# Kernel optimization log

Hardware: AMD Instinct MI355X
Metric: run time of the kernel (lower is better)

## Reference

```python
import jax, jax.numpy as jnp
import numpy as np

N, T, E = 20000, 4, 320000
IN_F, H_F, OUT_F, HEADS = 32, 16, 16, 8
NEG_SLOPE = 0.2


def gat_layer(x, W, al, ar, b, src, dst, n_nodes, heads, f_out):
    # x: [N, T, Fin], W: [Fin, heads*f_out], al/ar: [heads, f_out], b: [heads*f_out]
    feat = (x @ W).reshape(x.shape[0], x.shape[1], heads, f_out)      # [N,T,H,F]
    el = (feat * al).sum(-1)                                          # [N,T,H]
    er = (feat * ar).sum(-1)                                          # [N,T,H]
    e = jax.nn.leaky_relu(el[src] + er[dst], NEG_SLOPE)               # [E,T,H]
    # segment softmax over incoming edges of each destination node
    m = jax.lax.stop_gradient(jax.ops.segment_max(e, dst, num_segments=n_nodes))
    ex = jnp.exp(e - m[dst])
    s = jax.ops.segment_sum(ex, dst, num_segments=n_nodes)
    alpha = ex / s[dst]                                               # [E,T,H]
    msg = feat[src] * alpha[..., None]                                # [E,T,H,F]
    out = jax.ops.segment_sum(msg, dst, num_segments=n_nodes)
    return out + b.reshape(1, 1, heads, f_out)


def setup_inputs() -> dict:
    key = jax.random.key(0)
    ks = jax.random.split(key, 12)
    x = jax.random.normal(ks[0], (N, T, IN_F), dtype=jnp.float32)
    src = jax.random.randint(ks[1], (E,), 0, N)
    dst = jax.random.randint(ks[2], (E,), 0, N)
    s = 0.1
    W1 = jax.random.normal(ks[3], (IN_F, HEADS * H_F), dtype=jnp.float32) * s
    al1 = jax.random.normal(ks[4], (HEADS, H_F), dtype=jnp.float32) * s
    ar1 = jax.random.normal(ks[5], (HEADS, H_F), dtype=jnp.float32) * s
    b1 = jnp.zeros((HEADS * H_F,), dtype=jnp.float32)
    W2 = jax.random.normal(ks[6], (HEADS * H_F, OUT_F), dtype=jnp.float32) * s
    al2 = jax.random.normal(ks[7], (1, OUT_F), dtype=jnp.float32) * s
    ar2 = jax.random.normal(ks[8], (1, OUT_F), dtype=jnp.float32) * s
    b2 = jnp.zeros((OUT_F,), dtype=jnp.float32)
    return {"x": x, "src": src, "dst": dst, "W1": W1, "al1": al1, "ar1": ar1,
            "b1": b1, "W2": W2, "al2": al2, "ar2": ar2, "b2": b2}


def reference(x, src, dst, W1, al1, ar1, b1, W2, al2, ar2, b2):
    n = x.shape[0]
    h = gat_layer(x, W1, al1, ar1, b1, src, dst, n, HEADS, H_F)   # [N,T,H,F]
    h = h.reshape(n, h.shape[1], -1)                              # [N,T,H*F]
    h = gat_layer(h, W2, al2, ar2, b2, src, dst, n, 1, OUT_F)     # [N,T,1,OUT]
    return h.squeeze(2)                                           # [N,T,OUT]
```

## Files before the change

kernel.cpp:

```cpp
#include <hip/hip_runtime.h>
#include <hip/hip_fp16.h>
#include <math.h>

#define NN 20000
#define TT 4
#define EE 320000
#define NT (NN*TT)
#define H1 8
#define C1 128
#define IN_F 32
#define OUT_F 16
#define CAP 96

typedef _Float16 h8 __attribute__((ext_vector_type(8)));
typedef _Float16 h4v __attribute__((ext_vector_type(4)));
typedef float f32x4 __attribute__((ext_vector_type(4)));

__device__ __forceinline__ float lrelu_exp(float e) {
  e = (e >= 0.f) ? e : 0.2f * e;
  return __expf(e);
}

__global__ __launch_bounds__(256) void k_scatter_prep(
    const int4* __restrict__ src4, const int4* __restrict__ dst4,
    int* __restrict__ cnt, int* __restrict__ csr96,
    const float* __restrict__ W1, const float* __restrict__ al1,
    const float* __restrict__ ar1, const float* __restrict__ W2,
    const float* __restrict__ al2, const float* __restrict__ ar2,
    __half* __restrict__ W1p, __half* __restrict__ W2p) {
  int tid = threadIdx.x;
  int e4 = blockIdx.x * 256 + tid;
  if (e4 < EE / 4) {
    int4 s = src4[e4];
    int4 d = dst4[e4];
    int p0 = atomicAdd(&cnt[d.x], 1); csr96[d.x * CAP + p0] = s.x;
    int p1 = atomicAdd(&cnt[d.y], 1); csr96[d.y * CAP + p1] = s.y;
    int p2 = atomicAdd(&cnt[d.z], 1); csr96[d.z * CAP + p2] = s.z;
    int p3 = atomicAdd(&cnt[d.w], 1); csr96[d.w * CAP + p3] = s.w;
  }
  if (blockIdx.x == 0) {
    for (int idx = tid; idx < 9 * 512; idx += 256) {
      int tile = idx >> 9;
      int rem = idx & 511;
      int lane = rem >> 3, j = rem & 7;
      int k = (lane >> 4) * 8 + j;
      int n = lane & 15;
      float v;
      if (tile < 8) {
        v = W1[k * C1 + tile * 16 + n];
      } else {
        int hh = n & 7;
        const float* a = (n < 8) ? al1 : ar1;
        float s = 0.f;
        for (int f = 0; f < 16; ++f) s += W1[k * C1 + hh * 16 + f] * a[hh * 16 + f];
        v = s;
      }
      W1p[idx] = __float2half(v);
    }
    for (int idx = tid; idx < 8 * 512; idx += 256) {
      int tile = idx >> 9;
      int rem = idx & 511;
      int lane = rem >> 3, j = rem & 7;
      int ks = tile & 3;
      int k = ks * 32 + (lane >> 4) * 8 + j;
      int n = lane & 15;
      float v = 0.f;
      if (tile < 4) {
        v = W2[k * OUT_F + n];
      } else if (n == 0) {
        float s = 0.f;
        for (int f = 0; f < 16; ++f) s += W2[k * OUT_F + f] * al2[f];
        v = s;
      } else if (n == 1) {
        float s = 0.f;
        for (int f = 0; f < 16; ++f) s += W2[k * OUT_F + f] * ar2[f];
        v = s;
      }
      W2p[idx] = __float2half(v);
    }
  }
}

__global__ __launch_bounds__(256) void k_feat1(
    const float* __restrict__ x, const __half* __restrict__ W1p,
    __half* __restrict__ feat1h, float* __restrict__ el1, float* __restrict__ er1) {
  int tid = threadIdx.x;
  int wave = tid >> 6, lane = tid & 63;
  int m = lane & 15, quad = lane >> 4;
  int rowbase = blockIdx.x * 64 + wave * 16;
  int row = rowbase + m;
  const float4* xp = (const float4*)(x + row * IN_F + quad * 8);
  float4 a0 = xp[0], a1 = xp[1];
  h8 af;
  af[0] = (_Float16)a0.x; af[1] = (_Float16)a0.y;
  af[2] = (_Float16)a0.z; af[3] = (_Float16)a0.w;
  af[4] = (_Float16)a1.x; af[5] = (_Float16)a1.y;
  af[6] = (_Float16)a1.z; af[7] = (_Float16)a1.w;
  const h8* bp = (const h8*)W1p;
#pragma unroll
  for (int ht = 0; ht < 8; ++ht) {
    h8 bf = bp[ht * 64 + lane];
    f32x4 c = {0.f, 0.f, 0.f, 0.f};
    c = __builtin_amdgcn_mfma_f32_16x16x32_f16(af, bf, c, 0, 0, 0);
#pragma unroll
    for (int r = 0; r < 4; ++r)
      feat1h[(size_t)(rowbase + quad * 4 + r) * C1 + ht * 16 + m] = __float2half(c[r]);
  }
  {
    h8 bf = bp[8 * 64 + lane];
    f32x4 c = {0.f, 0.f, 0.f, 0.f};
    c = __builtin_amdgcn_mfma_f32_16x16x32_f16(af, bf, c, 0, 0, 0);
#pragma unroll
    for (int r = 0; r < 4; ++r) {
      int orow = rowbase + quad * 4 + r;
      if (m < 8) el1[orow * H1 + m] = c[r];
      else       er1[orow * H1 + (m - 8)] = c[r];
    }
  }
}

__global__ __launch_bounds__(256) void k_agg1(
    const __half* __restrict__ feat1h,
    const float* __restrict__ el1,
    const float* __restrict__ er1,
    const int* __restrict__ cnt, const int* __restrict__ csr96,
    const float* __restrict__ b1, __half* __restrict__ hh) {
  int tid = threadIdx.x;
  int wv = tid >> 6, lane = tid & 63;
  int n = blockIdx.x * 4 + wv;
  int ci = lane & 15;
  int i32 = lane & 31;
  int src_lane = ((lane >> 4) << 3) + (ci >> 1);
  float er_i = er1[(size_t)n * 32 + i32];
  int deg = cnt[n];
  const int* eb = csr96 + (size_t)n * CAP;
  float acc[8];
#pragma unroll
  for (int k = 0; k < 8; ++k) acc[k] = 0.f;
  float l = 0.f;
  for (int chunk = 0; chunk < deg; chunk += 64) {
    int m = min(64, deg - chunk);
    int sv = (lane < m) ? eb[chunk + lane] : 0;
    int iters = (m + 7) >> 3;
    for (int g = 0; g < iters; ++g) {
      int j = g * 8;
      int s0 = __builtin_amdgcn_readlane(sv, j + 0);
      int s1 = __builtin_amdgcn_readlane(sv, j + 1);
      int s2 = __builtin_amdgcn_readlane(sv, j + 2);
      int s3 = __builtin_amdgcn_readlane(sv, j + 3);
      int s4 = __builtin_amdgcn_readlane(sv, j + 4);
      int s5 = __builtin_amdgcn_readlane(sv, j + 5);
      int s6 = __builtin_amdgcn_readlane(sv, j + 6);
      int s7 = __builtin_amdgcn_readlane(sv, j + 7);
      float ew0 = el1[(size_t)s0 * 32 + i32];
      float ew1 = el1[(size_t)s1 * 32 + i32];
      float ew2 = el1[(size_t)s2 * 32 + i32];
      float ew3 = el1[(size_t)s3 * 32 + i32];
      float ew4 = el1[(size_t)s4 * 32 + i32];
      float ew5 = el1[(size_t)s5 * 32 + i32];
      float ew6 = el1[(size_t)s6 * 32 + i32];
      float ew7 = el1[(size_t)s7 * 32 + i32];
      h8 f0 = *(const h8*)(feat1h + (size_t)s0 * 512 + lane * 8);
      h8 f1 = *(const h8*)(feat1h + (size_t)s1 * 512 + lane * 8);
      h8 f2 = *(const h8*)(feat1h + (size_t)s2 * 512 + lane * 8);
      h8 f3 = *(const h8*)(feat1h + (size_t)s3 * 512 + lane * 8);
      h8 f4 = *(const h8*)(feat1h + (size_t)s4 * 512 + lane * 8);
      h8 f5 = *(const h8*)(feat1h + (size_t)s5 * 512 + lane * 8);
      h8 f6 = *(const h8*)(feat1h + (size_t)s6 * 512 + lane * 8);
      h8 f7 = *(const h8*)(feat1h + (size_t)s7 * 512 + lane * 8);
#define CONSUME(K, EW, F)                                         \
      {                                                           \
        float w_ = lrelu_exp(EW + er_i);                          \
        w_ = (j + K < m) ? w_ : 0.f;                              \
        float wb_ = __shfl(w_, src_lane);                         \
        l += wb_;                                                 \
        _Pragma("unroll")                                         \
        for (int q = 0; q < 8; ++q)                               \
          acc[q] = fmaf(wb_, (float)F[q], acc[q]);                \
      }
      CONSUME(0, ew0, f0) CONSUME(1, ew1, f1)
      CONSUME(2, ew2, f2) CONSUME(3, ew3, f3)
      CONSUME(4, ew4, f4) CONSUME(5, ew5, f5)
      CONSUME(6, ew6, f6) CONSUME(7, ew7, f7)
#undef CONSUME
    }
  }
  float inv = (l > 0.f) ? (1.f / l) : 0.f;
  float4 bv0 = *(const float4*)&b1[ci * 8];
  float4 bv1 = *(const float4*)&b1[ci * 8 + 4];
  h8 r;
  r[0] = (_Float16)(acc[0] * inv + bv0.x);
  r[1] = (_Float16)(acc[1] * inv + bv0.y);
  r[2] = (_Float16)(acc[2] * inv + bv0.z);
  r[3] = (_Float16)(acc[3] * inv + bv0.w);
  r[4] = (_Float16)(acc[4] * inv + bv1.x);
  r[5] = (_Float16)(acc[5] * inv + bv1.y);
  r[6] = (_Float16)(acc[6] * inv + bv1.z);
  r[7] = (_Float16)(acc[7] * inv + bv1.w);
  *(h8*)(hh + (size_t)n * 512 + lane * 8) = r;
}

__global__ __launch_bounds__(256) void k_feat2(
    const __half* __restrict__ hh, const __half* __restrict__ W2p,
    __half* __restrict__ feat2h, float* __restrict__ el2, float* __restrict__ er2) {
  int tid = threadIdx.x;
  int wave = tid >> 6, lane = tid & 63;
  int m = lane & 15, quad = lane >> 4;
  int rowbase = blockIdx.x * 64 + wave * 16;
  const h8* hp = (const h8*)hh;
  const h8* bp = (const h8*)W2p;
  f32x4 cF = {0.f, 0.f, 0.f, 0.f};
  f32x4 cE = {0.f, 0.f, 0.f, 0.f};
#pragma unroll
  for (int ks = 0; ks < 4; ++ks) {
    h8 af = hp[(size_t)(rowbase + m) * 16 + ks * 4 + quad];
    cF = __builtin_amdgcn_mfma_f32_16x16x32_f16(af, bp[ks * 64 + lane], cF, 0, 0, 0);
    cE = __builtin_amdgcn_mfma_f32_16x16x32_f16(af, bp[(4 + ks) * 64 + lane], cE, 0, 0, 0);
  }
#pragma unroll
  for (int r = 0; r < 4; ++r) {
    int orow = rowbase + quad * 4 + r;
    feat2h[(size_t)orow * OUT_F + m] = __float2half(cF[r]);
    if (m == 0) el2[orow] = cE[r];
    if (m == 1) er2[orow] = cE[r];
  }
}

__global__ __launch_bounds__(256) void k_agg2(
    const __half* __restrict__ feat2h,
    const float* __restrict__ el2, const float* __restrict__ er2,
    const int* __restrict__ cnt, const int* __restrict__ csr96,
    const float* __restrict__ b2, float* __restrict__ out) {
  __shared__ float myp[4][64][5];
  __shared__ int   svs[4][64];
  int tid = threadIdx.x;
  int wv = tid >> 6, lane = tid & 63;
  int n = blockIdx.x * 4 + wv;
  int e4 = lane >> 4, sub = lane & 15;
  int t = sub >> 2, fq = sub & 3;
  int deg = cnt[n];
  const int* eb = csr96 + (size_t)n * CAP;
  float4 ern = *(const float4*)&er2[n * TT];
  float acc[4] = {0.f, 0.f, 0.f, 0.f};
  float l = 0.f;
  for (int chunk = 0; chunk < deg; chunk += 64) {
    int m = min(64, deg - chunk);
    float4 w = {0.f, 0.f, 0.f, 0.f};
    int s = 0;
    if (lane < m) {
      s = eb[chunk + lane];
      float4 e = *(const float4*)&el2[s * TT];
      w.x = lrelu_exp(e.x + ern.x);
      w.y = lrelu_exp(e.y + ern.y);
      w.z = lrelu_exp(e.z + ern.z);
      w.w = lrelu_exp(e.w + ern.w);
    }
    svs[wv][lane] = s;
    myp[wv][lane][0] = w.x;
    myp[wv][lane][1] = w.y;
    myp[wv][lane][2] = w.z;
    myp[wv][lane][3] = w.w;
    int iters = (m + 3) >> 2;
    for (int g = 0; g < iters; ++g) {
      int jb = g * 4;
      int se = svs[wv][jb + e4];
      float we = myp[wv][jb + e4][t];
      h4v fv = *(const h4v*)(feat2h + (size_t)se * 64 + t * 16 + fq * 4);
      l += we;
      acc[0] = fmaf(we, (float)fv[0], acc[0]);
      acc[1] = fmaf(we, (float)fv[1], acc[1]);
      acc[2] = fmaf(we, (float)fv[2], acc[2]);
      acc[3] = fmaf(we, (float)fv[3], acc[3]);
    }
  }
#pragma unroll
  for (int mask = 16; mask <= 32; mask <<= 1) {
#pragma unroll
    for (int k = 0; k < 4; ++k) acc[k] += __shfl_xor(acc[k], mask);
    l += __shfl_xor(l, mask);
  }
  if (e4 == 0) {
    float inv = (l > 0.f) ? (1.f / l) : 0.f;
    float4 r;
    r.x = acc[0] * inv + b2[fq * 4 + 0];
    r.y = acc[1] * inv + b2[fq * 4 + 1];
    r.z = acc[2] * inv + b2[fq * 4 + 2];
    r.w = acc[3] * inv + b2[fq * 4 + 3];
    *(float4*)&out[(size_t)(n * TT + t) * OUT_F + fq * 4] = r;
  }
}

extern "C" void kernel_launch(void* const* d_in, const int* in_sizes, int n_in,
                              void* d_out, int out_size, void* d_ws, size_t ws_size,
                              hipStream_t stream) {
  const float* x   = (const float*)d_in[0];
  const int*   src = (const int*)d_in[1];
  const int*   dst = (const int*)d_in[2];
  const float* W1  = (const float*)d_in[3];
  const float* al1 = (const float*)d_in[4];
  const float* ar1 = (const float*)d_in[5];
  const float* b1  = (const float*)d_in[6];
  const float* W2  = (const float*)d_in[7];
  const float* al2 = (const float*)d_in[8];
  const float* ar2 = (const float*)d_in[9];
  const float* b2  = (const float*)d_in[10];
  float* out = (float*)d_out;

  char* w = (char*)d_ws;
  __half* feat1h = (__half*)w; w += (size_t)NT * C1 * 2;
  __half* hh     = (__half*)w; w += (size_t)NT * C1 * 2;
  __half* feat2h = (__half*)w; w += (size_t)NT * OUT_F * 2;
  float*  el1    = (float*)w;  w += (size_t)NT * H1 * 4;
  float*  er1    = (float*)w;  w += (size_t)NT * H1 * 4;
  float*  el2    = (float*)w;  w += (size_t)NT * 4;
  float*  er2    = (float*)w;  w += (size_t)NT * 4;
  __half* W1p    = (__half*)w; w += (size_t)9 * 512 * 2;
  __half* W2p    = (__half*)w; w += (size_t)8 * 512 * 2;
  int* cnt     = (int*)w;      w += (size_t)NN * 4;
  int* csr96   = (int*)w;      w += (size_t)NN * CAP * 4;

  hipMemsetAsync(cnt, 0, NN * sizeof(int), stream);

  k_scatter_prep<<<(EE / 4 + 255) / 256, 256, 0, stream>>>(
      (const int4*)src, (const int4*)dst, cnt, csr96,
      W1, al1, ar1, W2, al2, ar2, W1p, W2p);
  k_feat1<<<NT / 64, 256, 0, stream>>>(x, W1p, feat1h, el1, er1);
  k_agg1<<<NN / 4, 256, 0, stream>>>(feat1h, el1, er1, cnt, csr96, b1, hh);
  k_feat2<<<NT / 64, 256, 0, stream>>>(hh, W2p, feat2h, el2, er2);
  k_agg2<<<NN / 4, 256, 0, stream>>>(feat2h, el2, er2, cnt, csr96, b2, out);
}
```

Baseline: 181.0 us.

## Fuse edge scatter with layer-1 projection and fold layer-2 projection into aggregation

Merges the CSR scatter and the layer-1 feature projection into one launch, with blocks split by index, and has each block build packed W1 in shared memory. Folds the layer-2 projection into the layer-1 aggregation kernel: each wave keeps its node's hidden row in registers, shuffles it into MFMA operand layout and writes feat2/el2/er2 directly. This removes two kernel launches and the full 128-channel fp16 hidden-state round trip through global memory. In exchange every block recomputes the packed weight matrices, which adds redundant work and shared-memory use per block.

```diff
diff --git a/kernel.cpp b/kernel.cpp
--- a/kernel.cpp
+++ b/kernel.cpp
@@ -11,52 +11,108 @@
 #define IN_F 32
 #define OUT_F 16
 #define CAP 96
+#define SCAT_BLOCKS 313
+#define FEAT1_BLOCKS 1250
 
 typedef _Float16 h8 __attribute__((ext_vector_type(8)));
 typedef _Float16 h4v __attribute__((ext_vector_type(4)));
 typedef float f32x4 __attribute__((ext_vector_type(4)));
+typedef int i4v __attribute__((ext_vector_type(4)));
 
 __device__ __forceinline__ float lrelu_exp(float e) {
   e = (e >= 0.f) ? e : 0.2f * e;
   return __expf(e);
 }
 
-__global__ __launch_bounds__(256) void k_scatter_prep(
+__global__ __launch_bounds__(256) void k_front(
+    const float* __restrict__ x, const float* __restrict__ W1,
+    const float* __restrict__ al1, const float* __restrict__ ar1,
     const int4* __restrict__ src4, const int4* __restrict__ dst4,
     int* __restrict__ cnt, int* __restrict__ csr96,
-    const float* __restrict__ W1, const float* __restrict__ al1,
-    const float* __restrict__ ar1, const float* __restrict__ W2,
-    const float* __restrict__ al2, const float* __restrict__ ar2,
-    __half* __restrict__ W1p, __half* __restrict__ W2p) {
+    __half* __restrict__ feat1h, float* __restrict__ el1,
+    float* __restrict__ er1) {
+  __shared__ h8 W1ps[9 * 64];
+  int b = blockIdx.x;
   int tid = threadIdx.x;
-  int e4 = blockIdx.x * 256 + tid;
-  if (e4 < EE / 4) {
-    int4 s = src4[e4];
-    int4 d = dst4[e4];
-    int p0 = atomicAdd(&cnt[d.x], 1); csr96[d.x * CAP + p0] = s.x;
-    int p1 = atomicAdd(&cnt[d.y], 1); csr96[d.y * CAP + p1] = s.y;
-    int p2 = atomicAdd(&cnt[d.z], 1); csr96[d.z * CAP + p2] = s.z;
-    int p3 = atomicAdd(&cnt[d.w], 1); csr96[d.w * CAP + p3] = s.w;
-  }
-  if (blockIdx.x == 0) {
-    for (int idx = tid; idx < 9 * 512; idx += 256) {
-      int tile = idx >> 9;
-      int rem = idx & 511;
-      int lane = rem >> 3, j = rem & 7;
-      int k = (lane >> 4) * 8 + j;
-      int n = lane & 15;
-      float v;
-      if (tile < 8) {
-        v = W1[k * C1 + tile * 16 + n];
-      } else {
-        int hh = n & 7;
-        const float* a = (n < 8) ? al1 : ar1;
-        float s = 0.f;
-        for (int f = 0; f < 16; ++f) s += W1[k * C1 + hh * 16 + f] * a[hh * 16 + f];
-        v = s;
-      }
-      W1p[idx] = __float2half(v);
-    }
+  if (b < SCAT_BLOCKS) {
+    int e4 = b * 256 + tid;
+    if (e4 < EE / 4) {
+      int4 s = src4[e4];
+      int4 d = dst4[e4];
+      int p0 = atomicAdd(&cnt[d.x], 1); csr96[d.x * CAP + p0] = s.x;
+      int p1 = atomicAdd(&cnt[d.y], 1); csr96[d.y * CAP + p1] = s.y;
+      int p2 = atomicAdd(&cnt[d.z], 1); csr96[d.z * CAP + p2] = s.z;
+      int p3 = atomicAdd(&cnt[d.w], 1); csr96[d.w * CAP + p3] = s.w;
+    }
+    return;
+  }
+  __half* W1p = (__half*)W1ps;
+  for (int idx = tid; idx < 9 * 512; idx += 256) {
+    int tile = idx >> 9;
+    int rem = idx & 511;
+    int lane = rem >> 3, j = rem & 7;
+    int k = (lane >> 4) * 8 + j;
+    int n = lane & 15;
+    float v;
+    if (tile < 8) {
+      v = W1[k * C1 + tile * 16 + n];
+    } else {
+      int hh_ = n & 7;
+      const float* a = (n < 8) ? al1 : ar1;
+      float s = 0.f;
+      for (int f = 0; f < 16; ++f) s += W1[k * C1 + hh_ * 16 + f] * a[hh_ * 16 + f];
+      v = s;
+    }
+    W1p[idx] = __float2half(v);
+  }
+  __syncthreads();
+  int wave = tid >> 6, lane = tid & 63;
+  int m = lane & 15, quad = lane >> 4;
+  int rowbase = (b - SCAT_BLOCKS) * 64 + wave * 16;
+  int row = rowbase + m;
+  const float4* xp = (const float4*)(x + row * IN_F + quad * 8);
+  float4 a0 = xp[0], a1 = xp[1];
+  h8 af;
+  af[0] = (_Float16)a0.x; af[1] = (_Float16)a0.y;
+  af[2] = (_Float16)a0.z; af[3] = (_Float16)a0.w;
+  af[4] = (_Float16)a1.x; af[5] = (_Float16)a1.y;
+  af[6] = (_Float16)a1.z; af[7] = (_Float16)a1.w;
+#pragma unroll
+  for (int ht = 0; ht < 8; ++ht) {
+    h8 bf = W1ps[ht * 64 + lane];
+    f32x4 c = {0.f, 0.f, 0.f, 0.f};
+    c = __builtin_amdgcn_mfma_f32_16x16x32_f16(af, bf, c, 0, 0, 0);
+#pragma unroll
+    for (int r = 0; r < 4; ++r)
+      feat1h[(size_t)(rowbase + quad * 4 + r) * C1 + ht * 16 + m] = __float2half(c[r]);
+  }
+  {
+    h8 bf = W1ps[8 * 64 + lane];
+    f32x4 c = {0.f, 0.f, 0.f, 0.f};
+    c = __builtin_amdgcn_mfma_f32_16x16x32_f16(af, bf, c, 0, 0, 0);
+#pragma unroll
+    for (int r = 0; r < 4; ++r) {
+      int orow = rowbase + quad * 4 + r;
+      if (m < 8) el1[orow * H1 + m] = c[r];
+      else       er1[orow * H1 + (m - 8)] = c[r];
+    }
+  }
+}
+
+__global__ __launch_bounds__(256) void k_agg1f(
+    const __half* __restrict__ feat1h,
+    const float* __restrict__ el1,
+    const float* __restrict__ er1,
+    const int* __restrict__ cnt, const int* __restrict__ csr96,
+    const float* __restrict__ b1,
+    const float* __restrict__ W2, const float* __restrict__ al2,
+    const float* __restrict__ ar2,
+    __half* __restrict__ feat2h, float* __restrict__ el2,
+    float* __restrict__ er2) {
+  __shared__ h8 W2ps[8 * 64];
+  int tid = threadIdx.x;
+  {
+    __half* W2p = (__half*)W2ps;
     for (int idx = tid; idx < 8 * 512; idx += 256) {
       int tile = idx >> 9;
       int rem = idx & 511;
@@ -79,53 +135,8 @@
       W2p[idx] = __float2half(v);
     }
   }
-}
-
-__global__ __launch_bounds__(256) void k_feat1(
-    const float* __restrict__ x, const __half* __restrict__ W1p,
-    __half* __restrict__ feat1h, float* __restrict__ el1, float* __restrict__ er1) {
-  int tid = threadIdx.x;
-  int wave = tid >> 6, lane = tid & 63;
-  int m = lane & 15, quad = lane >> 4;
-  int rowbase = blockIdx.x * 64 + wave * 16;
-  int row = rowbase + m;
-  const float4* xp = (const float4*)(x + row * IN_F + quad * 8);
-  float4 a0 = xp[0], a1 = xp[1];
-  h8 af;
-  af[0] = (_Float16)a0.x; af[1] = (_Float16)a0.y;
-  af[2] = (_Float16)a0.z; af[3] = (_Float16)a0.w;
-  af[4] = (_Float16)a1.x; af[5] = (_Float16)a1.y;
-  af[6] = (_Float16)a1.z; af[7] = (_Float16)a1.w;
-  const h8* bp = (const h8*)W1p;
-#pragma unroll
-  for (int ht = 0; ht < 8; ++ht) {
-    h8 bf = bp[ht * 64 + lane];
-    f32x4 c = {0.f, 0.f, 0.f, 0.f};
-    c = __builtin_amdgcn_mfma_f32_16x16x32_f16(af, bf, c, 0, 0, 0);
-#pragma unroll
-    for (int r = 0; r < 4; ++r)
-      feat1h[(size_t)(rowbase + quad * 4 + r) * C1 + ht * 16 + m] = __float2half(c[r]);
-  }
-  {
-    h8 bf = bp[8 * 64 + lane];
-    f32x4 c = {0.f, 0.f, 0.f, 0.f};
-    c = __builtin_amdgcn_mfma_f32_16x16x32_f16(af, bf, c, 0, 0, 0);
-#pragma unroll
-    for (int r = 0; r < 4; ++r) {
-      int orow = rowbase + quad * 4 + r;
-      if (m < 8) el1[orow * H1 + m] = c[r];
-      else       er1[orow * H1 + (m - 8)] = c[r];
-    }
-  }
-}
-
-__global__ __launch_bounds__(256) void k_agg1(
-    const __half* __restrict__ feat1h,
-    const float* __restrict__ el1,
-    const float* __restrict__ er1,
-    const int* __restrict__ cnt, const int* __restrict__ csr96,
-    const float* __restrict__ b1, __half* __restrict__ hh) {
-  int tid = threadIdx.x;
+  __syncthreads();
+
   int wv = tid >> 6, lane = tid & 63;
   int n = blockIdx.x * 4 + wv;
   int ci = lane & 15;
@@ -197,32 +208,33 @@
   r[5] = (_Float16)(acc[5] * inv + bv1.y);
   r[6] = (_Float16)(acc[6] * inv + bv1.z);
   r[7] = (_Float16)(acc[7] * inv + bv1.w);
-  *(h8*)(hh + (size_t)n * 512 + lane * 8) = r;
-}
-
-__global__ __launch_bounds__(256) void k_feat2(
-    const __half* __restrict__ hh, const __half* __restrict__ W2p,
-    __half* __restrict__ feat2h, float* __restrict__ el2, float* __restrict__ er2) {
-  int tid = threadIdx.x;
-  int wave = tid >> 6, lane = tid & 63;
+
+  union U { h8 v; i4v d; };
+  U u; u.v = r;
   int m = lane & 15, quad = lane >> 4;
-  int rowbase = blockIdx.x * 64 + wave * 16;
-  const h8* hp = (const h8*)hh;
-  const h8* bp = (const h8*)W2p;
   f32x4 cF = {0.f, 0.f, 0.f, 0.f};
   f32x4 cE = {0.f, 0.f, 0.f, 0.f};
 #pragma unroll
   for (int ks = 0; ks < 4; ++ks) {
-    h8 af = hp[(size_t)(rowbase + m) * 16 + ks * 4 + quad];
-    cF = __builtin_amdgcn_mfma_f32_16x16x32_f16(af, bp[ks * 64 + lane], cF, 0, 0, 0);
-    cE = __builtin_amdgcn_mfma_f32_16x16x32_f16(af, bp[(4 + ks) * 64 + lane], cE, 0, 0, 0);
-  }
-#pragma unroll
-  for (int r = 0; r < 4; ++r) {
-    int orow = rowbase + quad * 4 + r;
-    feat2h[(size_t)orow * OUT_F + m] = __float2half(cF[r]);
-    if (m == 0) el2[orow] = cE[r];
-    if (m == 1) er2[orow] = cE[r];
+    int srcl = (m * 16 + ks * 4 + quad) & 63;
+    U a;
+#pragma unroll
+    for (int q = 0; q < 4; ++q) a.d[q] = __shfl(u.d[q], srcl);
+    cF = __builtin_amdgcn_mfma_f32_16x16x32_f16(a.v, W2ps[ks * 64 + lane], cF, 0, 0, 0);
+    cE = __builtin_amdgcn_mfma_f32_16x16x32_f16(a.v, W2ps[(4 + ks) * 64 + lane], cE, 0, 0, 0);
+  }
+  if (quad == 0) {
+#pragma unroll
+    for (int rr = 0; rr < 4; ++rr)
+      feat2h[(size_t)(n * 4 + rr) * OUT_F + m] = __float2half(cF[rr]);
+    if (m == 0) {
+      float4 v = {cE[0], cE[1], cE[2], cE[3]};
+      *(float4*)&el2[n * 4] = v;
+    }
+    if (m == 1) {
+      float4 v = {cE[0], cE[1], cE[2], cE[3]};
+      *(float4*)&er2[n * 4] = v;
+    }
   }
 }
 
@@ -308,24 +320,20 @@
 
   char* w = (char*)d_ws;
   __half* feat1h = (__half*)w; w += (size_t)NT * C1 * 2;
-  __half* hh     = (__half*)w; w += (size_t)NT * C1 * 2;
   __half* feat2h = (__half*)w; w += (size_t)NT * OUT_F * 2;
   float*  el1    = (float*)w;  w += (size_t)NT * H1 * 4;
   float*  er1    = (float*)w;  w += (size_t)NT * H1 * 4;
   float*  el2    = (float*)w;  w += (size_t)NT * 4;
   float*  er2    = (float*)w;  w += (size_t)NT * 4;
-  __half* W1p    = (__half*)w; w += (size_t)9 * 512 * 2;
-  __half* W2p    = (__half*)w; w += (size_t)8 * 512 * 2;
   int* cnt     = (int*)w;      w += (size_t)NN * 4;
   int* csr96   = (int*)w;      w += (size_t)NN * CAP * 4;
 
   hipMemsetAsync(cnt, 0, NN * sizeof(int), stream);
 
-  k_scatter_prep<<<(EE / 4 + 255) / 256, 256, 0, stream>>>(
-      (const int4*)src, (const int4*)dst, cnt, csr96,
-      W1, al1, ar1, W2, al2, ar2, W1p, W2p);
-  k_feat1<<<NT / 64, 256, 0, stream>>>(x, W1p, feat1h, el1, er1);
-  k_agg1<<<NN / 4, 256, 0, stream>>>(feat1h, el1, er1, cnt, csr96, b1, hh);
-  k_feat2<<<NT / 64, 256, 0, stream>>>(hh, W2p, feat2h, el2, er2);
+  k_front<<<SCAT_BLOCKS + FEAT1_BLOCKS, 256, 0, stream>>>(
+      x, W1, al1, ar1, (const int4*)src, (const int4*)dst, cnt, csr96,
+      feat1h, el1, er1);
+  k_agg1f<<<NN / 4, 256, 0, stream>>>(
+      feat1h, el1, er1, cnt, csr96, b1, W2, al2, ar2, feat2h, el2, er2);
   k_agg2<<<NN / 4, 256, 0, stream>>>(feat2h, el2, er2, cnt, csr96, b2, out);
 }
```

After: 204.1 us. 12.7% more time.
